# Performance work log

Hardware: AMD Instinct MI355X
Metric: run time of the kernel (lower is better)

Reference implementation:

```python
import jax, jax.numpy as jnp
import numpy as np


def setup_inputs() -> dict:
    key = jax.random.key(0)
    B, D, F = 8192, 768, 32768
    k_x, k_w = jax.random.split(key, 2)
    x = jax.random.normal(k_x, (B, D), dtype=jnp.float32)
    # xavier_normal init for W_enc: std = sqrt(2/(fan_in+fan_out))
    scale = (2.0 / (D + F)) ** 0.5
    W_enc = jax.random.normal(k_w, (D, F), dtype=jnp.float32) * scale
    # W_dec = W_enc.T with unit-norm rows (latent directions)
    W_dec = W_enc.T
    W_dec = W_dec / jnp.linalg.norm(W_dec, axis=1, keepdims=True)
    pre_bias = jnp.zeros((D,), dtype=jnp.float32)
    latent_bias = jnp.zeros((F,), dtype=jnp.float32)
    return {"x": x, "pre_bias": pre_bias, "W_enc": W_enc,
            "latent_bias": latent_bias, "W_dec": W_dec, "k": 32}


def reference(x, pre_bias, W_enc, latent_bias, W_dec, k):
    # encode: [B,F]
    latents_pre_act = (x - pre_bias) @ W_enc + latent_bias
    # topk selection then relu: relu(topk(pre_act, k))
    vals, idx = jax.lax.top_k(latents_pre_act, k)      # [B,k]
    vals = jax.nn.relu(vals)
    # sparse decode: gather only the k selected decoder rows per example
    # W_dec[idx]: [B,k,D]
    recons = jnp.einsum('bk,bkd->bd', vals, W_dec[idx]) + pre_bias
    return recons
```

## Files before the change

kernel.cpp:

```cpp
#include <hip/hip_runtime.h>
#include <stdint.h>

#define GAS __attribute__((address_space(1)))
#define LAS __attribute__((address_space(3)))

typedef __attribute__((ext_vector_type(8))) short bf16x8;
typedef __attribute__((ext_vector_type(4))) float f32x4;

static constexpr int NB = 8192;
static constexpr int DD = 768;
static constexpr int FF = 32768;
static constexpr int TK = 32;
static constexpr int RUNC = 48;
static constexpr int SLOT = 8;
static constexpr int NSEG = FF / 128;
static constexpr int SORTN = 1024;
static constexpr int NS2 = 256;
static constexpr int NKT = DD / 32;
static constexpr int PQ = 256 * 32;

__device__ __forceinline__ ushort f2bf(float f) {
    unsigned x = __float_as_uint(f);
    unsigned r = (x + 0x7FFFu + ((x >> 16) & 1u)) >> 16;
    return (ushort)r;
}
__device__ __forceinline__ ushort sortkey(ushort u) {
    return (u & 0x8000u) ? (ushort)(u ^ 0xFFFFu) : (ushort)(u | 0x8000u);
}
__device__ __forceinline__ float bf2f(ushort u) {
    return __uint_as_float(((unsigned)u) << 16);
}
__device__ __forceinline__ void gload_lds16(const void* g, void* l) {
    __builtin_amdgcn_global_load_lds((const GAS unsigned int*)g,
                                     (LAS unsigned int*)l, 16, 0, 0);
}
__device__ __forceinline__ size_t pan_off(int v, int d) {
    return ((size_t)(v >> 8) * NKT + (d >> 5)) * PQ + ((v & 255) << 5) + (d & 31);
}

__global__ __launch_bounds__(256) void prep_x_k(const float* __restrict__ x,
                                                const float* __restrict__ pb,
                                                ushort* __restrict__ Ap) {
    const int n4 = NB * DD / 4;
    for (int i = blockIdx.x * 256 + threadIdx.x; i < n4; i += gridDim.x * 256) {
        int b = i / (DD / 4), dq = (i % (DD / 4)) * 4;
        float4 v = ((const float4*)x)[i];
        float4 p = ((const float4*)pb)[i % (DD / 4)];
        ushort4 o;
        o.x = f2bf(v.x - p.x); o.y = f2bf(v.y - p.y);
        o.z = f2bf(v.z - p.z); o.w = f2bf(v.w - p.w);
        *(ushort4*)(Ap + pan_off(b, dq)) = o;
    }
}

__global__ __launch_bounds__(256) void prep_w_k(const float* __restrict__ W,
                                                ushort* __restrict__ Bp,
                                                float* __restrict__ Wt32,
                                                float* __restrict__ s2part) {
    __shared__ float tile[32][33];
    int f0 = blockIdx.x * 32, d0 = blockIdx.y * 32;
    int tx = threadIdx.x & 31, ty = threadIdx.x >> 5;
    float ss = 0.f;
#pragma unroll
    for (int q = 0; q < 4; q++) {
        int dl = ty + q * 8;
        float v = W[(size_t)(d0 + dl) * FF + f0 + tx];
        tile[dl][tx] = v;
        ss += v * v;
    }
#pragma unroll
    for (int o = 32; o >= 1; o >>= 1) ss += __shfl_down(ss, o);
    if ((threadIdx.x & 63) == 0) {
        int slot = (blockIdx.x * 97 + blockIdx.y * 13 + (threadIdx.x >> 6)) & (NS2 - 1);
        atomicAdd(&s2part[slot], ss);
    }
    __syncthreads();
#pragma unroll
    for (int q = 0; q < 4; q++) {
        int fl = ty + q * 8;
        float v = tile[tx][fl];
        int f = f0 + fl, d = d0 + tx;
        Bp[pan_off(f, d)] = f2bf(v);
        if (Wt32) Wt32[(size_t)f * DD + d] = v;
    }
}

__global__ __launch_bounds__(256) void rn_k(const float* __restrict__ x,
                                            const float* __restrict__ pb,
                                            const float* __restrict__ s2part,
                                            float* __restrict__ tau) {
    int t = threadIdx.x, l = t & 63, w = t >> 6;
    __shared__ float wsum[4];
    __shared__ float s2m;
    float p = s2part[t];
#pragma unroll
    for (int o = 32; o >= 1; o >>= 1) p += __shfl_down(p, o);
    if (l == 0) wsum[w] = p;
    __syncthreads();
    if (t == 0) s2m = (wsum[0] + wsum[1] + wsum[2] + wsum[3]) / ((float)DD * (float)FF);
    __syncthreads();
    int row = blockIdx.x * 4 + w;
    float ss = 0.f;
#pragma unroll
    for (int q = 0; q < 12; q++) {
        int d = l + 64 * q;
        float v = x[(size_t)row * DD + d] - pb[d];
        ss += v * v;
    }
#pragma unroll
    for (int o = 32; o >= 1; o >>= 1) ss += __shfl_down(ss, o);
    if (l == 0) tau[row] = 2.5f * sqrtf(s2m * ss);
}

#define MFMA16(A0, A1, A2, A3, MB)                                            \
    _Pragma("unroll")                                                         \
    for (int ni = 0; ni < 4; ni++) {                                          \
        acc[MB + 0][ni] = __builtin_amdgcn_mfma_f32_16x16x32_bf16(A0, bfr[ni], acc[MB + 0][ni], 0, 0, 0); \
        acc[MB + 1][ni] = __builtin_amdgcn_mfma_f32_16x16x32_bf16(A1, bfr[ni], acc[MB + 1][ni], 0, 0, 0); \
        acc[MB + 2][ni] = __builtin_amdgcn_mfma_f32_16x16x32_bf16(A2, bfr[ni], acc[MB + 2][ni], 0, 0, 0); \
        acc[MB + 3][ni] = __builtin_amdgcn_mfma_f32_16x16x32_bf16(A3, bfr[ni], acc[MB + 3][ni], 0, 0, 0); \
    }

__global__ __launch_bounds__(512, 2) void gemm_k(const ushort* __restrict__ Ap,
                                                 const ushort* __restrict__ Bp,
                                                 const float* __restrict__ lbias,
                                                 const float* __restrict__ tau,
                                                 unsigned* __restrict__ cand,
                                                 unsigned* __restrict__ rowbad) {
    __shared__ __align__(16) char smem[98304];

    int bid = (int)blockIdx.x;
    int wg = (bid & 7) * 512 + (bid >> 3);
    int mt = wg >> 7, nt = wg & 127;
    int m0 = mt << 8, n0 = nt << 8;

    int t = threadIdx.x, l = t & 63, w = t >> 6;
    int wm = w >> 2, wn = w & 3;

    int soff[4], ldo[4];
#pragma unroll
    for (int q = 0; q < 4; q++) {
        int s = q * 512 + t;
        int rr = (s & 1023) >> 2;
        int sl = (s & 3) ^ (rr & 3);
        soff[q] = rr * 32 + sl * 8;
        ldo[q] = s * 16;
    }
    const ushort* apan = Ap + (size_t)mt * NKT * PQ;
    const ushort* bpan = Bp + (size_t)nt * NKT * PQ;
    const ushort* sp0 = apan + soff[0];
    const ushort* sp1 = apan + soff[1];
    const ushort* sp2 = bpan + soff[2];
    const ushort* sp3 = bpan + soff[3];

    int xsl = ((l >> 4) ^ (l & 3)) << 4;
    int aro = (wm * 128 + (l & 15)) * 64 + xsl;
    int bro = (wn * 64 + (l & 15)) * 64 + xsl;

    f32x4 acc[8][4] = {};

    gload_lds16(sp0, smem + ldo[0]); gload_lds16(sp1, smem + ldo[1]);
    gload_lds16(sp2, smem + ldo[2]); gload_lds16(sp3, smem + ldo[3]);
    gload_lds16(sp0 + PQ, smem + 32768 + ldo[0]); gload_lds16(sp1 + PQ, smem + 32768 + ldo[1]);
    gload_lds16(sp2 + PQ, smem + 32768 + ldo[2]); gload_lds16(sp3 + PQ, smem + 32768 + ldo[3]);
    asm volatile("s_waitcnt vmcnt(0)" ::: "memory");
    __builtin_amdgcn_s_barrier();
    __builtin_amdgcn_sched_barrier(0);

    int cur = 0;
#pragma unroll 1
    for (int kt = 0; kt < NKT; kt++) {
        const char* Ar = smem + cur * 32768;
        const char* Br = Ar + 16384;
        int nxt = cur + 2; if (nxt >= 3) nxt -= 3;
        char* dst = smem + nxt * 32768;
        const size_t ko = (size_t)(kt + 2) * PQ;
        bool st = kt < NKT - 2;

        bf16x8 af0 = *(const bf16x8*)(Ar + aro);
        bf16x8 af1 = *(const bf16x8*)(Ar + aro + 1024);
        bf16x8 af2 = *(const bf16x8*)(Ar + aro + 2048);
        bf16x8 af3 = *(const bf16x8*)(Ar + aro + 3072);
        bf16x8 bfr[4];
        bfr[0] = *(const bf16x8*)(Br + bro);
        bfr[1] = *(const bf16x8*)(Br + bro + 1024);
        bfr[2] = *(const bf16x8*)(Br + bro + 2048);
        bfr[3] = *(const bf16x8*)(Br + bro + 3072);
        if (st) { gload_lds16(sp0 + ko, dst + ldo[0]); gload_lds16(sp1 + ko, dst + ldo[1]); }
        __builtin_amdgcn_s_barrier();
        __builtin_amdgcn_sched_barrier(0);
        __builtin_amdgcn_s_setprio(1);
        MFMA16(af0, af1, af2, af3, 0)
        __builtin_amdgcn_s_setprio(0);
        __builtin_amdgcn_s_barrier();
        __builtin_amdgcn_sched_barrier(0);

        bf16x8 af4 = *(const bf16x8*)(Ar + aro + 4096);
        bf16x8 af5 = *(const bf16x8*)(Ar + aro + 5120);
        bf16x8 af6 = *(const bf16x8*)(Ar + aro + 6144);
        bf16x8 af7 = *(const bf16x8*)(Ar + aro + 7168);
        if (st) {
            gload_lds16(sp2 + ko, dst + ldo[2]); gload_lds16(sp3 + ko, dst + ldo[3]);
            asm volatile("s_waitcnt vmcnt(4)" ::: "memory");
        } else {
            asm volatile("s_waitcnt vmcnt(0)" ::: "memory");
        }
        __builtin_amdgcn_s_barrier();
        __builtin_amdgcn_sched_barrier(0);
        __builtin_amdgcn_s_setprio(1);
        MFMA16(af4, af5, af6, af7, 4)
        __builtin_amdgcn_s_setprio(0);
        __builtin_amdgcn_s_barrier();
        __builtin_amdgcn_sched_barrier(0);

        cur = cur + 1; if (cur == 3) cur = 0;
    }

    int* lcnt = (int*)smem;
    unsigned* lbuf = (unsigned*)(smem + 2048);
    __syncthreads();
    lcnt[t] = 0;
    __syncthreads();
    float lbv[4]; int fcol[4];
#pragma unroll
    for (int ni = 0; ni < 4; ni++) {
        fcol[ni] = n0 + wn * 64 + ni * 16 + (l & 15);
        lbv[ni] = lbias[fcol[ni]];
    }
    int sh = wn >> 1;
#pragma unroll
    for (int mi = 0; mi < 8; mi++) {
        int rl = wm * 128 + mi * 16 + ((l >> 4) << 2);
        float4 tq = *(const float4*)(tau + m0 + rl);
        float tj[4] = {tq.x, tq.y, tq.z, tq.w};
#pragma unroll
        for (int ni = 0; ni < 4; ni++) {
            f32x4 v4 = acc[mi][ni];
#pragma unroll
            for (int j = 0; j < 4; j++) {
                float v = v4[j] + lbv[ni];
                if (v >= tj[j]) {
                    int idx = ((rl + j) << 1) + sh;
                    int p = atomicAdd(&lcnt[idx], 1);
                    if (p < SLOT)
                        lbuf[idx * SLOT + p] =
                            ((unsigned)sortkey(f2bf(v)) << 16) | (unsigned)(32767 - fcol[ni]);
                }
            }
        }
    }
    __syncthreads();
    {
        int row = t >> 1, sh2 = t & 1;
        int c = lcnt[t];
        int gr = m0 + row;
        if (c > SLOT) { atomicOr(&rowbad[gr], 1u); c = SLOT; }
        unsigned* dstc = cand + (size_t)gr * (NSEG * SLOT) + ((nt << 1) + sh2) * SLOT;
        for (int s2 = 0; s2 < c; s2++) dstc[s2] = lbuf[t * SLOT + s2];
    }
}

__global__ __launch_bounds__(256) void select2_k(const unsigned* __restrict__ cand,
                                                 const unsigned* __restrict__ rowbad,
                                                 unsigned* __restrict__ flagv,
                                                 int* __restrict__ ridx,
                                                 int* __restrict__ runcnt) {
    int b = blockIdx.x, t = threadIdx.x;
    __shared__ unsigned srt[SORTN];
    __shared__ int s_cnt;
    for (int i = t; i < SORTN; i += 256) srt[i] = 0;
    if (t == 0) s_cnt = 0;
    __syncthreads();
    const uint4* src = (const uint4*)(cand + (size_t)b * (NSEG * SLOT));
    for (int i = t; i < NSEG * SLOT / 4; i += 256) {
        uint4 v4 = src[i];
        unsigned d[4] = {v4.x, v4.y, v4.z, v4.w};
#pragma unroll
        for (int q = 0; q < 4; q++)
            if (d[q]) {
                int p = atomicAdd(&s_cnt, 1);
                if (p < SORTN) srt[p] = d[q];
            }
    }
    __syncthreads();
    int cnt = s_cnt;
    int bad = (rowbad[b] != 0u) || cnt < 48 || cnt > SORTN;
    if (t == 0) { flagv[b] = bad; if (bad) runcnt[b] = 0; }
    if (bad) return;
    for (int k = 2; k <= SORTN; k <<= 1) {
        for (int j = k >> 1; j > 0; j >>= 1) {
#pragma unroll
            for (int q = 0; q < SORTN / 256; q++) {
                int i = t + q * 256;
                int ixj = i ^ j;
                if (ixj > i) {
                    unsigned a = srt[i], c2 = srt[ixj];
                    bool sw = ((i & k) == 0) ? (a < c2) : (a > c2);
                    if (sw) { srt[i] = c2; srt[ixj] = a; }
                }
            }
            __syncthreads();
        }
    }
    int nc = cnt < RUNC ? cnt : RUNC;
    if (t < nc) ridx[(size_t)b * RUNC + t] = 32767 - (int)(srt[t] & 0xFFFFu);
    if (t == 0) runcnt[b] = nc;
}

__global__ __launch_bounds__(256) void fb_k(const unsigned* __restrict__ flagv,
                                            const float* __restrict__ x,
                                            const float* __restrict__ pb,
                                            const ushort* __restrict__ Bp,
                                            const float* __restrict__ lb,
                                            int* __restrict__ ridx,
                                            int* __restrict__ runcnt) {
    int b = blockIdx.x;
    if (!flagv[b]) return;
    int t = threadIdx.x;
    __shared__ float xs[DD];
    __shared__ unsigned hist[256];
    __shared__ int s_cb, s_cum, s_T, s_pos;
    for (int i = t; i < DD; i += 256) xs[i] = x[(size_t)b * DD + i] - pb[i];
    hist[t] = 0;
    if (t == 0) s_pos = 0;
    __syncthreads();
    for (int f = t; f < FF; f += 256) {
        float s = 0.f;
        for (int d = 0; d < DD; d++) s += xs[d] * bf2f(Bp[pan_off(f, d)]);
        ushort k = sortkey(f2bf(s + lb[f]));
        atomicAdd(&hist[k >> 8], 1u);
    }
    __syncthreads();
    if (t == 0) {
        int cum = 0, cb2 = 0;
        for (int i = 255; i >= 0; i--) {
            if (cum + (int)hist[i] >= 48) { cb2 = i; break; }
            cum += (int)hist[i];
        }
        s_cb = cb2; s_cum = cum;
    }
    __syncthreads();
    int cb2 = s_cb;
    hist[t] = 0;
    __syncthreads();
    for (int f = t; f < FF; f += 256) {
        float s = 0.f;
        for (int d = 0; d < DD; d++) s += xs[d] * bf2f(Bp[pan_off(f, d)]);
        ushort k = sortkey(f2bf(s + lb[f]));
        if ((int)(k >> 8) == cb2) atomicAdd(&hist[k & 0xFF], 1u);
    }
    __syncthreads();
    if (t == 0) {
        int cum = s_cum, T = cb2 << 8;
        for (int fb2 = 255; fb2 >= 0; fb2--) {
            if (cum + (int)hist[fb2] >= 48) { T = (cb2 << 8) | fb2; break; }
            cum += (int)hist[fb2];
        }
        s_T = T;
    }
    __syncthreads();
    unsigned T = (unsigned)s_T;
    for (int f = t; f < FF; f += 256) {
        float s = 0.f;
        for (int d = 0; d < DD; d++) s += xs[d] * bf2f(Bp[pan_off(f, d)]);
        ushort k = sortkey(f2bf(s + lb[f]));
        if (k >= T) {
            int p = atomicAdd(&s_pos, 1);
            if (p < RUNC) ridx[(size_t)b * RUNC + p] = f;
        }
    }
    __syncthreads();
    if (t == 0) runcnt[b] = s_pos < RUNC ? s_pos : RUNC;
}

__global__ __launch_bounds__(256) void refine_k(const float* __restrict__ x,
                                                const float* __restrict__ pb,
                                                const float* __restrict__ We,
                                                const float* __restrict__ Wt32,
                                                const float* __restrict__ lb,
                                                const int* __restrict__ runidx,
                                                const int* __restrict__ runcnt,
                                                int use_t,
                                                int* __restrict__ sidx,
                                                float* __restrict__ sval) {
    int b = blockIdx.x, t = threadIdx.x, l = t & 63, w = t >> 6;
    __shared__ float xs[DD];
    __shared__ int ci[RUNC];
    __shared__ float cv[RUNC];
    for (int i = t; i < DD; i += 256) xs[i] = x[(size_t)b * DD + i] - pb[i];
    int c = runcnt[b]; if (c > RUNC) c = RUNC;
    if (t < RUNC) cv[t] = -1e30f;
    if (t < c) ci[t] = runidx[(size_t)b * RUNC + t];
    __syncthreads();
    for (int j = w; j < c; j += 4) {
        int f = ci[j];
        double s = 0.0;
        if (use_t) {
            const float* wr = Wt32 + (size_t)f * DD;
#pragma unroll
            for (int q = 0; q < 12; q++)
                s = fma((double)wr[l + 64 * q], (double)xs[l + 64 * q], s);
        } else {
#pragma unroll
            for (int q = 0; q < 12; q++)
                s = fma((double)We[(size_t)(l + 64 * q) * FF + f], (double)xs[l + 64 * q], s);
        }
#pragma unroll
        for (int o = 32; o >= 1; o >>= 1) s += __shfl_down(s, o);
        if (l == 0) cv[j] = (float)(s + (double)lb[f]);
    }
    __syncthreads();
    if (w == 0) {
        float v0 = (l < RUNC) ? cv[l] : -1e30f;
        int i0 = (l < c) ? ci[l] : 0x7FFFFFFF;
        for (int sel = 0; sel < TK; sel++) {
            float bv = v0; int bi = i0;
#pragma unroll
            for (int o = 32; o >= 1; o >>= 1) {
                float ov = __shfl_xor(bv, o);
                int oi = __shfl_xor(bi, o);
                if (ov > bv || (ov == bv && oi < bi)) { bv = ov; bi = oi; }
            }
            if (i0 == bi) v0 = -1e30f;
            if (l == 0) {
                if (bi == 0x7FFFFFFF) { bi = 0; bv = -1e30f; }
                sidx[(size_t)b * TK + sel] = bi;
                sval[(size_t)b * TK + sel] = bv > 0.f ? bv : 0.f;
            }
        }
    }
}

__global__ __launch_bounds__(192) void decode_k(const float* __restrict__ sval,
                                                const int* __restrict__ sidx,
                                                const float* __restrict__ Wd,
                                                const float* __restrict__ pb,
                                                float* __restrict__ out) {
    int b = blockIdx.x, t = threadIdx.x;
    __shared__ float sv[TK];
    __shared__ int si[TK];
    if (t < TK) { sv[t] = sval[(size_t)b * TK + t]; si[t] = sidx[(size_t)b * TK + t]; }
    __syncthreads();
    float4 acc = ((const float4*)pb)[t];
#pragma unroll 4
    for (int j = 0; j < TK; j++) {
        float v = sv[j];
        float4 wv = ((const float4*)(Wd + (size_t)si[j] * DD))[t];
        acc.x += v * wv.x; acc.y += v * wv.y;
        acc.z += v * wv.z; acc.w += v * wv.w;
    }
    ((float4*)out)[(size_t)b * (DD / 4) + t] = acc;
}

extern "C" void kernel_launch(void* const* d_in, const int* in_sizes, int n_in,
                              void* d_out, int out_size, void* d_ws, size_t ws_size,
                              hipStream_t stream) {
    const float* x  = (const float*)d_in[0];
    const float* pb = (const float*)d_in[1];
    const float* We = (const float*)d_in[2];
    const float* lb = (const float*)d_in[3];
    const float* Wd = (const float*)d_in[4];
    float* out = (float*)d_out;
    char* ws = (char*)d_ws;
    (void)in_sizes; (void)n_in; (void)out_size;

    const size_t SZ_AP   = (size_t)NB * DD * 2;
    const size_t SZ_BP   = (size_t)FF * DD * 2;
    const size_t SZ_WT32 = (size_t)FF * DD * 4;
    const size_t SZ_CAND = (size_t)NB * NSEG * SLOT * 4;
    const size_t SZ_TAU  = (size_t)NB * 4;
    const size_t SZ_RIDX = (size_t)NB * RUNC * 4;
    const size_t SZ_RCNT = (size_t)NB * 4;
    const size_t SZ_SIDX = (size_t)NB * TK * 4;
    const size_t SZ_SVAL = (size_t)NB * TK * 4;
    const size_t SZ_CTRL = (size_t)NB * 4 + NS2 * 4 + SZ_CAND;

    size_t need_base = SZ_AP + SZ_BP + SZ_CTRL + (size_t)NB * 4 +
                       SZ_TAU + SZ_RIDX + SZ_RCNT + SZ_SIDX + SZ_SVAL;
    int use_t = (ws_size >= need_base + SZ_WT32) ? 1 : 0;

    size_t off = 0;
    ushort* Ap    = (ushort*)(ws + off); off += SZ_AP;
    ushort* Bp    = (ushort*)(ws + off); off += SZ_BP;
    float*  Wt32  = nullptr;
    if (use_t) { Wt32 = (float*)(ws + off); off += SZ_WT32; }
    char* ctrl0   = (char*)(ws + off);
    unsigned* rowbad = (unsigned*)(ws + off); off += (size_t)NB * 4;
    float* s2part = (float*)(ws + off); off += NS2 * 4;
    unsigned* cand = (unsigned*)(ws + off); off += SZ_CAND;
    size_t ctrl_bytes = (size_t)((ws + off) - ctrl0);
    unsigned* flagv = (unsigned*)(ws + off); off += (size_t)NB * 4;
    float* tau    = (float*)(ws + off); off += SZ_TAU;
    int* ridx     = (int*)(ws + off); off += SZ_RIDX;
    int* rcnt     = (int*)(ws + off); off += SZ_RCNT;
    int* sidx     = (int*)(ws + off); off += SZ_SIDX;
    float* sval   = (float*)(ws + off); off += SZ_SVAL;

    hipMemsetAsync(ctrl0, 0, ctrl_bytes, stream);
    prep_x_k<<<2048, 256, 0, stream>>>(x, pb, Ap);
    prep_w_k<<<dim3(FF / 32, DD / 32), 256, 0, stream>>>(We, Bp, Wt32, s2part);
    rn_k<<<NB / 4, 256, 0, stream>>>(x, pb, s2part, tau);
    gemm_k<<<(NB / 256) * (FF / 256), 512, 0, stream>>>(Ap, Bp, lb, tau, cand, rowbad);
    select2_k<<<NB, 256, 0, stream>>>(cand, rowbad, flagv, ridx, rcnt);
    fb_k<<<NB, 256, 0, stream>>>(flagv, x, pb, Bp, lb, ridx, rcnt);
    refine_k<<<NB, 256, 0, stream>>>(x, pb, We, Wt32, lb, ridx, rcnt, use_t, sidx, sval);
    decode_k<<<NB, 192, 0, stream>>>(sval, sidx, Wd, pb, out);
}
```

Baseline: 1.111 ms.

## Shrink GEMM tile to 128x128 with 256-thread blocks and simpler pipeline

Reworks the encoder GEMM from 256x256 tiles with 512 threads into 128x128 tiles with 256 threads and three blocks per CU. The panel layout, LDS staging, swizzle removal and candidate-slot indexing all change to match. The aim is higher occupancy and a simpler single-phase MFMA loop. In exchange, each tile reuses less data, so global traffic rises. Dropping the LDS XOR swizzle may also cause bank conflicts on fragment reads.

```diff
diff --git a/kernel.cpp b/kernel.cpp
--- a/kernel.cpp
+++ b/kernel.cpp
@@ -17,7 +17,7 @@
 static constexpr int SORTN = 1024;
 static constexpr int NS2 = 256;
 static constexpr int NKT = DD / 32;
-static constexpr int PQ = 256 * 32;
+static constexpr int PQ = 128 * 32;
 
 __device__ __forceinline__ ushort f2bf(float f) {
     unsigned x = __float_as_uint(f);
@@ -35,7 +35,7 @@
                                      (LAS unsigned int*)l, 16, 0, 0);
 }
 __device__ __forceinline__ size_t pan_off(int v, int d) {
-    return ((size_t)(v >> 8) * NKT + (d >> 5)) * PQ + ((v & 255) << 5) + (d & 31);
+    return ((size_t)(v >> 7) * NKT + (d >> 5)) * PQ + ((v & 127) << 5) + (d & 31);
 }
 
 __global__ __launch_bounds__(256) void prep_x_k(const float* __restrict__ x,
@@ -112,114 +112,89 @@
     if (l == 0) tau[row] = 2.5f * sqrtf(s2m * ss);
 }
 
-#define MFMA16(A0, A1, A2, A3, MB)                                            \
-    _Pragma("unroll")                                                         \
-    for (int ni = 0; ni < 4; ni++) {                                          \
-        acc[MB + 0][ni] = __builtin_amdgcn_mfma_f32_16x16x32_bf16(A0, bfr[ni], acc[MB + 0][ni], 0, 0, 0); \
-        acc[MB + 1][ni] = __builtin_amdgcn_mfma_f32_16x16x32_bf16(A1, bfr[ni], acc[MB + 1][ni], 0, 0, 0); \
-        acc[MB + 2][ni] = __builtin_amdgcn_mfma_f32_16x16x32_bf16(A2, bfr[ni], acc[MB + 2][ni], 0, 0, 0); \
-        acc[MB + 3][ni] = __builtin_amdgcn_mfma_f32_16x16x32_bf16(A3, bfr[ni], acc[MB + 3][ni], 0, 0, 0); \
-    }
-
-__global__ __launch_bounds__(512, 2) void gemm_k(const ushort* __restrict__ Ap,
+__global__ __launch_bounds__(256, 3) void gemm_k(const ushort* __restrict__ Ap,
                                                  const ushort* __restrict__ Bp,
                                                  const float* __restrict__ lbias,
                                                  const float* __restrict__ tau,
                                                  unsigned* __restrict__ cand,
                                                  unsigned* __restrict__ rowbad) {
-    __shared__ __align__(16) char smem[98304];
+    __shared__ __align__(16) char smem[49152];
 
     int bid = (int)blockIdx.x;
-    int wg = (bid & 7) * 512 + (bid >> 3);
-    int mt = wg >> 7, nt = wg & 127;
-    int m0 = mt << 8, n0 = nt << 8;
+    int wg = (bid & 7) * 2048 + (bid >> 3);
+    int mt = wg >> 8, nt = wg & 255;
+    int m0 = mt << 7, n0 = nt << 7;
 
     int t = threadIdx.x, l = t & 63, w = t >> 6;
-    int wm = w >> 2, wn = w & 3;
-
-    int soff[4], ldo[4];
-#pragma unroll
-    for (int q = 0; q < 4; q++) {
-        int s = q * 512 + t;
-        int rr = (s & 1023) >> 2;
-        int sl = (s & 3) ^ (rr & 3);
-        soff[q] = rr * 32 + sl * 8;
-        ldo[q] = s * 16;
-    }
-    const ushort* apan = Ap + (size_t)mt * NKT * PQ;
-    const ushort* bpan = Bp + (size_t)nt * NKT * PQ;
-    const ushort* sp0 = apan + soff[0];
-    const ushort* sp1 = apan + soff[1];
-    const ushort* sp2 = bpan + soff[2];
-    const ushort* sp3 = bpan + soff[3];
-
-    int xsl = ((l >> 4) ^ (l & 3)) << 4;
-    int aro = (wm * 128 + (l & 15)) * 64 + xsl;
-    int bro = (wn * 64 + (l & 15)) * 64 + xsl;
-
-    f32x4 acc[8][4] = {};
-
-    gload_lds16(sp0, smem + ldo[0]); gload_lds16(sp1, smem + ldo[1]);
-    gload_lds16(sp2, smem + ldo[2]); gload_lds16(sp3, smem + ldo[3]);
-    gload_lds16(sp0 + PQ, smem + 32768 + ldo[0]); gload_lds16(sp1 + PQ, smem + 32768 + ldo[1]);
-    gload_lds16(sp2 + PQ, smem + 32768 + ldo[2]); gload_lds16(sp3 + PQ, smem + 32768 + ldo[3]);
-    asm volatile("s_waitcnt vmcnt(0)" ::: "memory");
+    int wm = w >> 1, wn = w & 1;
+
+    const ushort* sA = Ap + (size_t)mt * NKT * PQ + t * 8;
+    const ushort* sB = Bp + (size_t)nt * NKT * PQ + t * 8;
+    int ldA = t * 16, ldB = 8192 + t * 16;
+
+    int aro = (wm * 64 + (l & 15)) * 64 + ((l >> 4) << 4);
+    int bro = (wn * 64 + (l & 15)) * 64 + ((l >> 4) << 4);
+
+    f32x4 acc[4][4] = {};
+
+#define STAGE(slot, kt)                                                       \
+    {                                                                         \
+        const size_t o = (size_t)(kt) * PQ;                                   \
+        char* base = smem + (slot) * 16384;                                   \
+        gload_lds16(sA + o, base + ldA);                                      \
+        gload_lds16(sA + o + 2048, base + ldA + 4096);                        \
+        gload_lds16(sB + o, base + ldB);                                      \
+        gload_lds16(sB + o + 2048, base + ldB + 4096);                        \
+    }
+
+    STAGE(0, 0)
+    STAGE(1, 1)
+    asm volatile("s_waitcnt vmcnt(4)" ::: "memory");
     __builtin_amdgcn_s_barrier();
     __builtin_amdgcn_sched_barrier(0);
 
     int cur = 0;
 #pragma unroll 1
     for (int kt = 0; kt < NKT; kt++) {
-        const char* Ar = smem + cur * 32768;
-        const char* Br = Ar + 16384;
+        const char* As = smem + cur * 16384;
+        const char* Bs = As + 8192;
         int nxt = cur + 2; if (nxt >= 3) nxt -= 3;
-        char* dst = smem + nxt * 32768;
-        const size_t ko = (size_t)(kt + 2) * PQ;
-        bool st = kt < NKT - 2;
-
-        bf16x8 af0 = *(const bf16x8*)(Ar + aro);
-        bf16x8 af1 = *(const bf16x8*)(Ar + aro + 1024);
-        bf16x8 af2 = *(const bf16x8*)(Ar + aro + 2048);
-        bf16x8 af3 = *(const bf16x8*)(Ar + aro + 3072);
-        bf16x8 bfr[4];
-        bfr[0] = *(const bf16x8*)(Br + bro);
-        bfr[1] = *(const bf16x8*)(Br + bro + 1024);
-        bfr[2] = *(const bf16x8*)(Br + bro + 2048);
-        bfr[3] = *(const bf16x8*)(Br + bro + 3072);
-        if (st) { gload_lds16(sp0 + ko, dst + ldo[0]); gload_lds16(sp1 + ko, dst + ldo[1]); }
+        if (kt < NKT - 2) STAGE(nxt, kt + 2)
+
+        bf16x8 af[4], bfr[4];
+        af[0]  = *(const bf16x8*)(As + aro);
+        af[1]  = *(const bf16x8*)(As + aro + 1024);
+        af[2]  = *(const bf16x8*)(As + aro + 2048);
+        af[3]  = *(const bf16x8*)(As + aro + 3072);
+        bfr[0] = *(const bf16x8*)(Bs + bro);
+        bfr[1] = *(const bf16x8*)(Bs + bro + 1024);
+        bfr[2] = *(const bf16x8*)(Bs + bro + 2048);
+        bfr[3] = *(const bf16x8*)(Bs + bro + 3072);
+        asm volatile("s_waitcnt lgkmcnt(0)" ::: "memory");
+        __builtin_amdgcn_sched_barrier(0);
+        __builtin_amdgcn_s_setprio(1);
+#pragma unroll
+        for (int mi = 0; mi < 4; mi++)
+#pragma unroll
+            for (int ni = 0; ni < 4; ni++)
+                acc[mi][ni] = __builtin_amdgcn_mfma_f32_16x16x32_bf16(
+                    af[mi], bfr[ni], acc[mi][ni], 0, 0, 0);
+        __builtin_amdgcn_s_setprio(0);
+        __builtin_amdgcn_sched_barrier(0);
+        if (kt < NKT - 2)
+            asm volatile("s_waitcnt vmcnt(4)" ::: "memory");
+        else
+            asm volatile("s_waitcnt vmcnt(0)" ::: "memory");
         __builtin_amdgcn_s_barrier();
         __builtin_amdgcn_sched_barrier(0);
-        __builtin_amdgcn_s_setprio(1);
-        MFMA16(af0, af1, af2, af3, 0)
-        __builtin_amdgcn_s_setprio(0);
-        __builtin_amdgcn_s_barrier();
-        __builtin_amdgcn_sched_barrier(0);
-
-        bf16x8 af4 = *(const bf16x8*)(Ar + aro + 4096);
-        bf16x8 af5 = *(const bf16x8*)(Ar + aro + 5120);
-        bf16x8 af6 = *(const bf16x8*)(Ar + aro + 6144);
-        bf16x8 af7 = *(const bf16x8*)(Ar + aro + 7168);
-        if (st) {
-            gload_lds16(sp2 + ko, dst + ldo[2]); gload_lds16(sp3 + ko, dst + ldo[3]);
-            asm volatile("s_waitcnt vmcnt(4)" ::: "memory");
-        } else {
-            asm volatile("s_waitcnt vmcnt(0)" ::: "memory");
-        }
-        __builtin_amdgcn_s_barrier();
-        __builtin_amdgcn_sched_barrier(0);
-        __builtin_amdgcn_s_setprio(1);
-        MFMA16(af4, af5, af6, af7, 4)
-        __builtin_amdgcn_s_setprio(0);
-        __builtin_amdgcn_s_barrier();
-        __builtin_amdgcn_sched_barrier(0);
-
         cur = cur + 1; if (cur == 3) cur = 0;
     }
-
+#undef STAGE
+
+    __syncthreads();
     int* lcnt = (int*)smem;
-    unsigned* lbuf = (unsigned*)(smem + 2048);
-    __syncthreads();
-    lcnt[t] = 0;
+    unsigned* lbuf = (unsigned*)(smem + 512);
+    if (t < 128) lcnt[t] = 0;
     __syncthreads();
     float lbv[4]; int fcol[4];
 #pragma unroll
@@ -227,10 +202,9 @@
         fcol[ni] = n0 + wn * 64 + ni * 16 + (l & 15);
         lbv[ni] = lbias[fcol[ni]];
     }
-    int sh = wn >> 1;
-#pragma unroll
-    for (int mi = 0; mi < 8; mi++) {
-        int rl = wm * 128 + mi * 16 + ((l >> 4) << 2);
+#pragma unroll
+    for (int mi = 0; mi < 4; mi++) {
+        int rl = wm * 64 + mi * 16 + ((l >> 4) << 2);
         float4 tq = *(const float4*)(tau + m0 + rl);
         float tj[4] = {tq.x, tq.y, tq.z, tq.w};
 #pragma unroll
@@ -240,7 +214,7 @@
             for (int j = 0; j < 4; j++) {
                 float v = v4[j] + lbv[ni];
                 if (v >= tj[j]) {
-                    int idx = ((rl + j) << 1) + sh;
+                    int idx = rl + j;
                     int p = atomicAdd(&lcnt[idx], 1);
                     if (p < SLOT)
                         lbuf[idx * SLOT + p] =
@@ -250,12 +224,11 @@
         }
     }
     __syncthreads();
-    {
-        int row = t >> 1, sh2 = t & 1;
+    if (t < 128) {
         int c = lcnt[t];
-        int gr = m0 + row;
+        int gr = m0 + t;
         if (c > SLOT) { atomicOr(&rowbad[gr], 1u); c = SLOT; }
-        unsigned* dstc = cand + (size_t)gr * (NSEG * SLOT) + ((nt << 1) + sh2) * SLOT;
+        unsigned* dstc = cand + (size_t)gr * (NSEG * SLOT) + nt * SLOT;
         for (int s2 = 0; s2 < c; s2++) dstc[s2] = lbuf[t * SLOT + s2];
     }
 }
@@ -500,7 +473,7 @@
     prep_x_k<<<2048, 256, 0, stream>>>(x, pb, Ap);
     prep_w_k<<<dim3(FF / 32, DD / 32), 256, 0, stream>>>(We, Bp, Wt32, s2part);
     rn_k<<<NB / 4, 256, 0, stream>>>(x, pb, s2part, tau);
-    gemm_k<<<(NB / 256) * (FF / 256), 512, 0, stream>>>(Ap, Bp, lb, tau, cand, rowbad);
+    gemm_k<<<(NB / 128) * (FF / 128), 256, 0, stream>>>(Ap, Bp, lb, tau, cand, rowbad);
     select2_k<<<NB, 256, 0, stream>>>(cand, rowbad, flagv, ridx, rcnt);
     fb_k<<<NB, 256, 0, stream>>>(flagv, x, pb, Bp, lb, ridx, rcnt);
     refine_k<<<NB, 256, 0, stream>>>(x, pb, We, Wt32, lb, ridx, rcnt, use_t, sidx, sval);
```

After: 1.059 ms. 4.7% less time.
